# Kernel tuning notes

Measured on AMD Instinct MI355X. Metric: run time of the kernel, lower is better.

Reference implementation:

```python
import jax, jax.numpy as jnp
import numpy as np

NUM_HEADS = 16
BN_EPS = 1e-5


def setup_inputs() -> dict:
    key = jax.random.key(0)
    ks = jax.random.split(key, 12)
    B, S, D = 8, 1024, 1024
    s = 1.0 / np.sqrt(D)
    return {
        "key": jax.random.normal(ks[0], (B, S, D), jnp.float32),
        "value": jax.random.normal(ks[1], (B, S, D), jnp.float32),
        "query": jax.random.normal(ks[2], (B, S, D), jnp.float32),
        "Wk": jax.random.normal(ks[3], (D, D), jnp.float32) * s,
        "bk": jax.random.normal(ks[4], (D,), jnp.float32) * s,
        "Wv": jax.random.normal(ks[5], (D, D), jnp.float32) * s,
        "bv": jax.random.normal(ks[6], (D,), jnp.float32) * s,
        "Wq": jax.random.normal(ks[7], (D, D), jnp.float32) * s,
        "bq": jax.random.normal(ks[8], (D,), jnp.float32) * s,
        "Wf": jax.random.normal(ks[9], (D, D), jnp.float32) * s,
        "bf": jax.random.normal(ks[10], (D,), jnp.float32) * s,
        "gamma": jnp.ones((D,), jnp.float32),
        "beta": jnp.zeros((D,), jnp.float32),
    }


def _mha(key, value, query, Wk, bk, Wv, bv, Wq, bq, Wf, bf, gamma, beta):
    B, S, D = query.shape
    H = NUM_HEADS
    d = D // H
    residual = query

    k = key @ Wk + bk      # [B, S, D]
    v = value @ Wv + bv
    q = query @ Wq + bq

    # Faithful to torch: raw row-major view(B*H, -1, d) — NOT the standard head transpose.
    k = k.reshape(B * H, -1, d)   # [B*H, S, d]
    v = v.reshape(B * H, -1, d)
    q = q.reshape(B * H, -1, d)

    # Faithful quirky scale: (dim_per_head // num_heads) ** -0.5
    scale = jnp.float32((d // H) ** (-0.5))

    scores = jnp.einsum('bqd,bkd->bqk', q, k) * scale          # [B*H, S, S]
    attention = jax.nn.softmax(scores, axis=2)
    context = jnp.einsum('bqk,bkd->bqd', attention, v)          # [B*H, S, d]

    context = context.reshape(B, -1, D)                         # [B, S, D]
    out = context @ Wf + bf

    # BatchNorm1d over channel dim D (training mode: batch stats over B and S, biased var)
    x = residual + out                                          # [B, S, D]
    mean = jnp.mean(x, axis=(0, 1))
    var = jnp.mean((x - mean) ** 2, axis=(0, 1))
    out = (x - mean) * jax.lax.rsqrt(var + BN_EPS) * gamma + beta
    return out, attention


def reference(key, value, query, Wk, bk, Wv, bv, Wq, bq, Wf, bf, gamma, beta):
    return _mha(key, value, query, Wk, bk, Wv, bv, Wq, bq, Wf, bf, gamma, beta)
```

## Files before the change

kernel.cpp:

```cpp
#include <hip/hip_runtime.h>
#include <hip/hip_bf16.h>
#include <stdint.h>

typedef __attribute__((ext_vector_type(8))) short     short8;
typedef __attribute__((ext_vector_type(8))) _Float16  f16x8;
typedef __attribute__((ext_vector_type(4))) float     f32x4;
typedef __attribute__((ext_vector_type(8))) unsigned short ushort8;
typedef __attribute__((ext_vector_type(4))) unsigned short ushort4_t;

__device__ inline unsigned short f2bf(float f) {
    unsigned u = __float_as_uint(f);
    u += 0x7fffu + ((u >> 16) & 1u);
    return (unsigned short)(u >> 16);
}
__device__ inline float bf2f(unsigned short h) {
    return __uint_as_float(((unsigned)h) << 16);
}
__device__ inline unsigned short f2h(float f) {
    _Float16 h = (_Float16)f;
    unsigned short r;
    __builtin_memcpy(&r, &h, 2);
    return r;
}

__device__ inline void gload16(const void* g, void* lds) {
    unsigned loff = (unsigned)(uintptr_t)lds;
    loff = __builtin_amdgcn_readfirstlane(loff);
    auto l = (__attribute__((address_space(3))) unsigned int*)(uintptr_t)loff;
    auto p = (const __attribute__((address_space(1))) unsigned int*)(uintptr_t)g;
    __builtin_amdgcn_global_load_lds(p, l, 16, 0, 0);
}

__global__ void cvt3_f32_2b(const float4* __restrict__ k, const float4* __restrict__ q,
                            const float4* __restrict__ v,
                            ushort4_t* __restrict__ k16, ushort4_t* __restrict__ q16,
                            ushort4_t* __restrict__ v16, int n4) {
    const int which = blockIdx.y;
    const float4* in  = which == 0 ? k   : which == 1 ? q   : v;
    ushort4_t*    out = which == 0 ? k16 : which == 1 ? q16 : v16;
    const bool tof16 = (which < 2);
    for (int i = blockIdx.x * blockDim.x + threadIdx.x; i < n4; i += gridDim.x * blockDim.x) {
        float4 vv = in[i];
        ushort4_t r;
        if (tof16) { r.x = f2h(vv.x);  r.y = f2h(vv.y);  r.z = f2h(vv.z);  r.w = f2h(vv.w); }
        else       { r.x = f2bf(vv.x); r.y = f2bf(vv.y); r.z = f2bf(vv.z); r.w = f2bf(vv.w); }
        out[i] = r;
    }
}

template<int TOF16>
__global__ void transpose_cvt(const float* __restrict__ W, unsigned short* __restrict__ WT, int dim) {
    __shared__ float t[32][33];
    const int bx = blockIdx.x * 32, by = blockIdx.y * 32;
    const int tx = threadIdx.x, ty = threadIdx.y;
#pragma unroll
    for (int i = 0; i < 4; ++i)
        t[ty + 8 * i][tx] = W[(size_t)(by + ty + 8 * i) * dim + bx + tx];
    __syncthreads();
#pragma unroll
    for (int i = 0; i < 4; ++i) {
        float v = t[tx][ty + 8 * i];
        WT[(size_t)(bx + ty + 8 * i) * dim + by + tx] = TOF16 ? f2h(v) : f2bf(v);
    }
}

__global__ void transpose_v(const unsigned short* __restrict__ v, unsigned short* __restrict__ vT) {
    const int bh = blockIdx.z, d0 = blockIdx.x * 32, s0 = blockIdx.y * 32;
    __shared__ unsigned short t[32][33];
    const int tx = threadIdx.x, ty = threadIdx.y;
    const size_t base = (size_t)bh << 16;
#pragma unroll
    for (int i = 0; i < 4; ++i)
        t[ty + 8 * i][tx] = v[base + (size_t)(s0 + ty + 8 * i) * 64 + d0 + tx];
    __syncthreads();
#pragma unroll
    for (int i = 0; i < 4; ++i)
        vT[base + (size_t)(d0 + ty + 8 * i) * 1024 + s0 + tx] = t[tx][ty + 8 * i];
}

template<int F16IN, int EPI>
__global__ __launch_bounds__(256, 2) void gemm_bt(
    const unsigned short* __restrict__ A,
    const unsigned short* __restrict__ Bt,
    const float* __restrict__ bias,
    unsigned short* __restrict__ C2b,
    const float* __restrict__ resid,
    float* __restrict__ Cf,
    int M, int N, int K, int nbx)
{
    const int bid = blockIdx.x;
    const int cpx = gridDim.x >> 3;
    const int swz = (bid & 7) * cpx + (bid >> 3);
    const int bm = swz / nbx, bn = swz % nbx;
    const int m0 = bm * 128, n0 = bn * 128;

    const int tid = threadIdx.x;
    const int w = tid >> 6, l = tid & 63, g = l >> 4, c = l & 15;
    const int wr = w >> 1, wc = w & 1;

    __shared__ unsigned short As[4096];
    __shared__ unsigned short Bs[4096];

    f32x4 acc[4][4] = {};

    const int arow = tid >> 2, acol = (tid & 3) * 8;
    const unsigned short* Ap  = A  + (size_t)(m0 + arow) * K + acol;
    const unsigned short* Ap2 = A  + (size_t)(m0 + 64 + arow) * K + acol;
    const unsigned short* Bp  = Bt + (size_t)(n0 + arow) * K + acol;
    const unsigned short* Bp2 = Bt + (size_t)(n0 + 64 + arow) * K + acol;
    unsigned short* AsW  = &As[w * 512];
    unsigned short* AsW2 = &As[2048 + w * 512];
    unsigned short* BsW  = &Bs[w * 512];
    unsigned short* BsW2 = &Bs[2048 + w * 512];

    for (int k0 = 0; k0 < K; k0 += 32) {
        gload16(Ap + k0,  AsW);
        gload16(Ap2 + k0, AsW2);
        gload16(Bp + k0,  BsW);
        gload16(Bp2 + k0, BsW2);
        asm volatile("s_waitcnt vmcnt(0)" ::: "memory");
        __syncthreads();

        if constexpr (F16IN) {
            f16x8 a[4], b[4];
#pragma unroll
            for (int mt = 0; mt < 4; ++mt)
                a[mt] = *(const f16x8*)&As[(wr * 64 + mt * 16 + c) * 32 + g * 8];
#pragma unroll
            for (int nt = 0; nt < 4; ++nt)
                b[nt] = *(const f16x8*)&Bs[(wc * 64 + nt * 16 + c) * 32 + g * 8];
#pragma unroll
            for (int mt = 0; mt < 4; ++mt)
#pragma unroll
                for (int nt = 0; nt < 4; ++nt)
                    acc[mt][nt] = __builtin_amdgcn_mfma_f32_16x16x32_f16(a[mt], b[nt], acc[mt][nt], 0, 0, 0);
        } else {
            short8 a[4], b[4];
#pragma unroll
            for (int mt = 0; mt < 4; ++mt)
                a[mt] = *(const short8*)&As[(wr * 64 + mt * 16 + c) * 32 + g * 8];
#pragma unroll
            for (int nt = 0; nt < 4; ++nt)
                b[nt] = *(const short8*)&Bs[(wc * 64 + nt * 16 + c) * 32 + g * 8];
#pragma unroll
            for (int mt = 0; mt < 4; ++mt)
#pragma unroll
                for (int nt = 0; nt < 4; ++nt)
                    acc[mt][nt] = __builtin_amdgcn_mfma_f32_16x16x32_bf16(a[mt], b[nt], acc[mt][nt], 0, 0, 0);
        }
        __syncthreads();
    }

#pragma unroll
    for (int nt = 0; nt < 4; ++nt) {
        const int col = n0 + wc * 64 + nt * 16 + c;
        const float bs = bias[col];
#pragma unroll
        for (int mt = 0; mt < 4; ++mt) {
            const int row0 = m0 + wr * 64 + mt * 16 + g * 4;
#pragma unroll
            for (int r = 0; r < 4; ++r) {
                const float x = acc[mt][nt][r] + bs;
                const size_t idx = (size_t)(row0 + r) * N + col;
                if constexpr (EPI == 0) {
                    C2b[idx] = F16IN ? f2h(x) : f2bf(x);
                } else {
                    Cf[idx] = x + resid[idx];
                }
            }
        }
    }
}

__global__ __launch_bounds__(256, 4) void attn_kernel(
    const unsigned short* __restrict__ qf,
    const unsigned short* __restrict__ kf,
    const unsigned short* __restrict__ vT,
    float* __restrict__ attn_out,
    unsigned short* __restrict__ ctx)
{
    const int L = blockIdx.x;
    const int rb = (L >> 3) & 63;
    const int bh = ((L & 7) << 4) | (L >> 9);

    const int tid = threadIdx.x;
    const int w = tid >> 6, l = tid & 63, g = l >> 4, c = l & 15;
    const int n0 = w * 256;

    __shared__ unsigned short P[16 * 1024];
    __shared__ float rs_lds[4][16];
    __shared__ float inv_lds[16];

    const unsigned short* qb = qf + ((size_t)bh << 16) + (size_t)(rb * 16 + c) * 64 + g * 8;
    const f16x8 q0 = *(const f16x8*)(qb);
    const f16x8 q1 = *(const f16x8*)(qb + 32);

    const unsigned short* kb = kf + ((size_t)bh << 16);
    const unsigned swzc = ((unsigned)(c & 7)) << 4;
    const unsigned prow = (unsigned)c * 2048;

    ushort4_t pks[16];
    float rsum = 0.f;

#pragma unroll
    for (int t = 0; t < 16; ++t) {
        const unsigned short* kp = kb + (size_t)(n0 + t * 16 + c) * 64 + g * 8;
        const f16x8 a0 = *(const f16x8*)(kp);
        const f16x8 a1 = *(const f16x8*)(kp + 32);
        f32x4 s = {0.f, 0.f, 0.f, 0.f};
        s = __builtin_amdgcn_mfma_f32_16x16x32_f16(a0, q0, s, 0, 0, 0);
        s = __builtin_amdgcn_mfma_f32_16x16x32_f16(a1, q1, s, 0, 0, 0);

        const float p0 = __expf(s[0] * 0.5f);
        const float p1 = __expf(s[1] * 0.5f);
        const float p2 = __expf(s[2] * 0.5f);
        const float p3 = __expf(s[3] * 0.5f);
        rsum += (p0 + p1) + (p2 + p3);

        ushort4_t pk;
        pk.x = f2bf(p0); pk.y = f2bf(p1); pk.z = f2bf(p2); pk.w = f2bf(p3);
        pks[t] = pk;
        *(ushort4_t*)((char*)P + ((prow + (unsigned)(n0 * 2 + t * 32 + g * 8)) ^ swzc)) = pk;
    }

    rsum += __shfl_xor(rsum, 16);
    rsum += __shfl_xor(rsum, 32);
    if (g == 0) rs_lds[w][c] = rsum;
    __syncthreads();
    if (tid < 16)
        inv_lds[tid] = 1.0f / (rs_lds[0][tid] + rs_lds[1][tid] + rs_lds[2][tid] + rs_lds[3][tid]);
    __syncthreads();

    const float inv = inv_lds[c];
    float* ao = attn_out + ((size_t)bh << 20) + (size_t)(rb * 16 + c) * 1024 + n0 + g * 4;
    f32x4 pacc = {0.f, 0.f, 0.f, 0.f};
    const unsigned short* vb = vT + ((size_t)bh << 16) + (size_t)(w * 16 + c) * 1024;
#pragma unroll
    for (int ks = 0; ks < 32; ++ks) {
        const short8 a = *(const short8*)((char*)P + ((prow + (unsigned)(ks * 64 + g * 16)) ^ swzc));
        const short8 b = *(const short8*)(vb + ks * 32 + g * 8);
        pacc = __builtin_amdgcn_mfma_f32_16x16x32_bf16(a, b, pacc, 0, 0, 0);
        if (ks & 1) {
            const int t = ks >> 1;
            const ushort4_t pk = pks[t];
            f32x4 o;
            o[0] = bf2f(pk.x) * inv;
            o[1] = bf2f(pk.y) * inv;
            o[2] = bf2f(pk.z) * inv;
            o[3] = bf2f(pk.w) * inv;
            __builtin_nontemporal_store(o, (f32x4*)(ao + t * 16));
        }
    }
    unsigned short* cb = ctx + ((size_t)bh << 16) + (size_t)(rb * 16) * 64 + w * 16 + c;
#pragma unroll
    for (int r = 0; r < 4; ++r) {
        const int row = g * 4 + r;
        cb[(size_t)row * 64] = f2bf(pacc[r] * inv_lds[row]);
    }
}

__global__ void bn_stats(const float* __restrict__ x, float* __restrict__ psum, float* __restrict__ psq) {
    const int col = blockIdx.y * 256 + threadIdx.x;
    const int r0 = blockIdx.x * 128;
    float s = 0.f, q = 0.f;
#pragma unroll 4
    for (int r = 0; r < 128; ++r) {
        const float v = x[(size_t)(r0 + r) * 1024 + col];
        s += v; q += v * v;
    }
    psum[blockIdx.x * 1024 + col] = s;
    psq [blockIdx.x * 1024 + col] = q;
}

__global__ void bn_final(const float* __restrict__ psum, const float* __restrict__ psq,
                         const float* __restrict__ gamma, const float* __restrict__ beta,
                         float* __restrict__ ab) {
    const int cidx = threadIdx.x;
    float s = 0.f, q = 0.f;
#pragma unroll 8
    for (int i = 0; i < 64; ++i) { s += psum[i * 1024 + cidx]; q += psq[i * 1024 + cidx]; }
    const float mean = s * (1.0f / 8192.0f);
    const float var  = q * (1.0f / 8192.0f) - mean * mean;
    const float a = gamma[cidx] * rsqrtf(var + 1e-5f);
    ab[cidx]        = a;
    ab[1024 + cidx] = beta[cidx] - mean * a;
}

__global__ void bn_apply(const float4* __restrict__ x4, const float* __restrict__ ab, float4* __restrict__ o4) {
    const int n4 = 2 * 1024 * 1024;
    for (int i = blockIdx.x * blockDim.x + threadIdx.x; i < n4; i += gridDim.x * blockDim.x) {
        const float4 v = x4[i];
        const int c0 = (i & 255) << 2;
        float4 r;
        r.x = v.x * ab[c0 + 0] + ab[1024 + c0 + 0];
        r.y = v.y * ab[c0 + 1] + ab[1024 + c0 + 1];
        r.z = v.z * ab[c0 + 2] + ab[1024 + c0 + 2];
        r.w = v.w * ab[c0 + 3] + ab[1024 + c0 + 3];
        o4[i] = r;
    }
}

extern "C" void kernel_launch(void* const* d_in, const int* in_sizes, int n_in,
                              void* d_out, int out_size, void* d_ws, size_t ws_size,
                              hipStream_t stream) {
    (void)in_sizes; (void)n_in; (void)out_size; (void)ws_size;

    const float* key   = (const float*)d_in[0];
    const float* value = (const float*)d_in[1];
    const float* query = (const float*)d_in[2];
    const float* Wk = (const float*)d_in[3];
    const float* bk = (const float*)d_in[4];
    const float* Wv = (const float*)d_in[5];
    const float* bv = (const float*)d_in[6];
    const float* Wq = (const float*)d_in[7];
    const float* bq = (const float*)d_in[8];
    const float* Wf = (const float*)d_in[9];
    const float* bff = (const float*)d_in[10];
    const float* gamma = (const float*)d_in[11];
    const float* beta  = (const float*)d_in[12];

    char* ws = (char*)d_ws;
    const size_t MB = 1u << 20;
    unsigned short* key16   = (unsigned short*)(ws + 0);
    unsigned short* ctx     = (unsigned short*)(ws + 0);
    unsigned short* query16 = (unsigned short*)(ws + 16 * MB);
    unsigned short* value16 = (unsigned short*)(ws + 32 * MB);
    float*          xbuf    = (float*)(ws + 16 * MB);
    unsigned short* WkT = (unsigned short*)(ws + 48 * MB);
    unsigned short* WqT = (unsigned short*)(ws + 50 * MB);
    unsigned short* WvT = (unsigned short*)(ws + 52 * MB);
    unsigned short* WfT = (unsigned short*)(ws + 54 * MB);
    unsigned short* kbuf = (unsigned short*)(ws + 56 * MB);
    unsigned short* qbuf = (unsigned short*)(ws + 72 * MB);
    unsigned short* vbuf = (unsigned short*)(ws + 88 * MB);
    float* psum = (float*)(ws + 88 * MB);
    float* psq  = (float*)(ws + 88 * MB + 256 * 1024);
    float* ab   = (float*)(ws + 88 * MB + 512 * 1024);
    unsigned short* vTbuf = (unsigned short*)(ws + 104 * MB);

    float* out0 = (float*)d_out;
    float* attn = out0 + 8388608;

    const int n4big = 2 * 1024 * 1024;

    cvt3_f32_2b<<<dim3(1024, 3), 256, 0, stream>>>(
        (const float4*)key, (const float4*)query, (const float4*)value,
        (ushort4_t*)key16, (ushort4_t*)query16, (ushort4_t*)value16, n4big);

    dim3 tb(32, 8), tg(32, 32);
    transpose_cvt<1><<<tg, tb, 0, stream>>>(Wk, WkT, 1024);
    transpose_cvt<1><<<tg, tb, 0, stream>>>(Wq, WqT, 1024);
    transpose_cvt<0><<<tg, tb, 0, stream>>>(Wv, WvT, 1024);
    transpose_cvt<0><<<tg, tb, 0, stream>>>(Wf, WfT, 1024);

    gemm_bt<1, 0><<<512, 256, 0, stream>>>(key16,   WkT, bk, kbuf, nullptr, nullptr, 8192, 1024, 1024, 8);
    gemm_bt<1, 0><<<512, 256, 0, stream>>>(query16, WqT, bq, qbuf, nullptr, nullptr, 8192, 1024, 1024, 8);
    gemm_bt<0, 0><<<512, 256, 0, stream>>>(value16, WvT, bv, vbuf, nullptr, nullptr, 8192, 1024, 1024, 8);

    transpose_v<<<dim3(2, 32, 128), tb, 0, stream>>>(vbuf, vTbuf);

    attn_kernel<<<8192, 256, 0, stream>>>(qbuf, kbuf, vTbuf, attn, ctx);

    gemm_bt<0, 1><<<512, 256, 0, stream>>>(ctx, WfT, bff, nullptr, query, xbuf, 8192, 1024, 1024, 8);

    bn_stats<<<dim3(64, 4), 256, 0, stream>>>(xbuf, psum, psq);
    bn_final<<<1, 1024, 0, stream>>>(psum, psq, gamma, beta, ab);
    bn_apply<<<2048, 256, 0, stream>>>((const float4*)xbuf, ab, (float4*)out0);
}
```

Baseline: 458.9 us.

## Double-buffer GEMM shared-memory tiles to overlap global loads with MFMA

Splits the A/B shared-memory tiles into two buffers and issues the next K-slice's global-to-LDS loads before computing on the current slice. It waits only for the older loads (vmcnt(4)), so memory latency can overlap with MFMA work instead of stalling every iteration. The cost is twice the LDS per block, which may lower occupancy, plus sched_barriers that restrict compiler reordering.

```diff
diff --git a/kernel.cpp b/kernel.cpp
--- a/kernel.cpp
+++ b/kernel.cpp
@@ -98,8 +98,8 @@
     const int w = tid >> 6, l = tid & 63, g = l >> 4, c = l & 15;
     const int wr = w >> 1, wc = w & 1;
 
-    __shared__ unsigned short As[4096];
-    __shared__ unsigned short Bs[4096];
+    __shared__ unsigned short As[2][4096];
+    __shared__ unsigned short Bs[2][4096];
 
     f32x4 acc[4][4] = {};
 
@@ -108,48 +108,68 @@
     const unsigned short* Ap2 = A  + (size_t)(m0 + 64 + arow) * K + acol;
     const unsigned short* Bp  = Bt + (size_t)(n0 + arow) * K + acol;
     const unsigned short* Bp2 = Bt + (size_t)(n0 + 64 + arow) * K + acol;
-    unsigned short* AsW  = &As[w * 512];
-    unsigned short* AsW2 = &As[2048 + w * 512];
-    unsigned short* BsW  = &Bs[w * 512];
-    unsigned short* BsW2 = &Bs[2048 + w * 512];
-
-    for (int k0 = 0; k0 < K; k0 += 32) {
-        gload16(Ap + k0,  AsW);
-        gload16(Ap2 + k0, AsW2);
-        gload16(Bp + k0,  BsW);
-        gload16(Bp2 + k0, BsW2);
-        asm volatile("s_waitcnt vmcnt(0)" ::: "memory");
-        __syncthreads();
-
-        if constexpr (F16IN) {
-            f16x8 a[4], b[4];
-#pragma unroll
-            for (int mt = 0; mt < 4; ++mt)
-                a[mt] = *(const f16x8*)&As[(wr * 64 + mt * 16 + c) * 32 + g * 8];
-#pragma unroll
-            for (int nt = 0; nt < 4; ++nt)
-                b[nt] = *(const f16x8*)&Bs[(wc * 64 + nt * 16 + c) * 32 + g * 8];
-#pragma unroll
-            for (int mt = 0; mt < 4; ++mt)
-#pragma unroll
-                for (int nt = 0; nt < 4; ++nt)
-                    acc[mt][nt] = __builtin_amdgcn_mfma_f32_16x16x32_f16(a[mt], b[nt], acc[mt][nt], 0, 0, 0);
-        } else {
-            short8 a[4], b[4];
-#pragma unroll
-            for (int mt = 0; mt < 4; ++mt)
-                a[mt] = *(const short8*)&As[(wr * 64 + mt * 16 + c) * 32 + g * 8];
-#pragma unroll
-            for (int nt = 0; nt < 4; ++nt)
-                b[nt] = *(const short8*)&Bs[(wc * 64 + nt * 16 + c) * 32 + g * 8];
-#pragma unroll
-            for (int mt = 0; mt < 4; ++mt)
-#pragma unroll
-                for (int nt = 0; nt < 4; ++nt)
-                    acc[mt][nt] = __builtin_amdgcn_mfma_f32_16x16x32_bf16(a[mt], b[nt], acc[mt][nt], 0, 0, 0);
-        }
-        __syncthreads();
-    }
+
+    const int NT = K >> 5;
+
+#define STAGE_GEMM(bufi, koff)                                   \
+    do {                                                         \
+        gload16(Ap  + (koff), &As[bufi][w * 512]);               \
+        gload16(Ap2 + (koff), &As[bufi][2048 + w * 512]);        \
+        gload16(Bp  + (koff), &Bs[bufi][w * 512]);               \
+        gload16(Bp2 + (koff), &Bs[bufi][2048 + w * 512]);        \
+    } while (0)
+
+#define COMPUTE_GEMM(bufi)                                                         \
+    do {                                                                           \
+        if constexpr (F16IN) {                                                     \
+            f16x8 a[4], b[4];                                                      \
+            _Pragma("unroll")                                                      \
+            for (int mt = 0; mt < 4; ++mt)                                         \
+                a[mt] = *(const f16x8*)&As[bufi][(wr * 64 + mt * 16 + c) * 32 + g * 8]; \
+            _Pragma("unroll")                                                      \
+            for (int nt = 0; nt < 4; ++nt)                                         \
+                b[nt] = *(const f16x8*)&Bs[bufi][(wc * 64 + nt * 16 + c) * 32 + g * 8]; \
+            _Pragma("unroll")                                                      \
+            for (int mt = 0; mt < 4; ++mt)                                         \
+                _Pragma("unroll")                                                  \
+                for (int nt = 0; nt < 4; ++nt)                                     \
+                    acc[mt][nt] = __builtin_amdgcn_mfma_f32_16x16x32_f16(a[mt], b[nt], acc[mt][nt], 0, 0, 0); \
+        } else {                                                                   \
+            short8 a[4], b[4];                                                     \
+            _Pragma("unroll")                                                      \
+            for (int mt = 0; mt < 4; ++mt)                                         \
+                a[mt] = *(const short8*)&As[bufi][(wr * 64 + mt * 16 + c) * 32 + g * 8]; \
+            _Pragma("unroll")                                                      \
+            for (int nt = 0; nt < 4; ++nt)                                         \
+                b[nt] = *(const short8*)&Bs[bufi][(wc * 64 + nt * 16 + c) * 32 + g * 8]; \
+            _Pragma("unroll")                                                      \
+            for (int mt = 0; mt < 4; ++mt)                                         \
+                _Pragma("unroll")                                                  \
+                for (int nt = 0; nt < 4; ++nt)                                     \
+                    acc[mt][nt] = __builtin_amdgcn_mfma_f32_16x16x32_bf16(a[mt], b[nt], acc[mt][nt], 0, 0, 0); \
+        }                                                                          \
+    } while (0)
+
+    STAGE_GEMM(0, 0);
+
+#pragma unroll 2
+    for (int kt = 0; kt < NT - 1; ++kt) {
+        const int cur = kt & 1;
+        STAGE_GEMM(cur ^ 1, (kt + 1) * 32);
+        asm volatile("s_waitcnt vmcnt(4)" ::: "memory");
+        __builtin_amdgcn_s_barrier();
+        __builtin_amdgcn_sched_barrier(0);
+        COMPUTE_GEMM(cur);
+        __builtin_amdgcn_sched_barrier(0);
+        __builtin_amdgcn_s_barrier();
+    }
+    asm volatile("s_waitcnt vmcnt(0)" ::: "memory");
+    __builtin_amdgcn_s_barrier();
+    __builtin_amdgcn_sched_barrier(0);
+    COMPUTE_GEMM((NT - 1) & 1);
+
+#undef STAGE_GEMM
+#undef COMPUTE_GEMM
 
 #pragma unroll
     for (int nt = 0; nt < 4; ++nt) {
```

New measurement: 445.6 us, median of 2. 1.03x faster.
